# Optimization experiments

Measured on AMD Instinct MI355X. Metric: run time of the kernel, lower is better.

## Reference

```python
import jax, jax.numpy as jnp
import numpy as np

N = 50000      # nodes
E = 800000     # edges (avg degree 16)
F = 32         # n_features
FOUT = 32      # n_features_out
L = 2          # n_layers (Message+Update pairs)
LEN = 10.0     # length_scale


def _mlp(x, w1, b1, w2, b2):
    # embedding.MLP: Linear -> SiLU -> Linear
    return jax.nn.silu(x @ w1 + b1) @ w2 + b2


def _posenc(d):
    # sinusoidal PositionalEncoder(F, length=LEN): ranks 1..F/2
    ranks = jnp.arange(1, F // 2 + 1, dtype=d.dtype)
    a = d[:, None] * ranks * (jnp.pi / LEN)           # [E, F/2]
    return jnp.concatenate([jnp.sin(a), jnp.cos(a)], axis=-1)  # [E, F]


def _painn(s, v, edge_index, edge_dist, edge_dir,
           mp_w1, mp_b1, mp_w2, mp_b2, mw_w1, mw_b1, mw_w2, mw_b2,
           u_U, u_V, u_w1, u_b1, u_w2, u_b2,
           ro_w1, ro_b1, ro_w2, ro_b2, ro_V):
    src, dst = edge_index[0], edge_index[1]
    pe = _posenc(edge_dist)                            # [E, F]
    dirb = edge_dir[:, None, :]                        # [E, 1, 3]
    for l in range(L):
        # ---- Message ----
        mix = _mlp(s[src], mp_w1[l], mp_b1[l], mp_w2[l], mp_b2[l]) \
            * _mlp(pe, mw_w1[l], mw_b1[l], mw_w2[l], mw_b2[l])     # [E, 4F]
        gates, cpg, sed, sf = jnp.split(mix, 4, axis=-1)
        cross = jnp.cross(dirb, v[dst])                # [E, F, 3] (broadcast)
        dv = sed[:, :, None] * dirb + gates[:, :, None] * v[src] \
           + cpg[:, :, None] * cross                   # [E, F, 3]
        ds = sf * s[src]                               # [E, F]
        v = v + jax.ops.segment_sum(dv, dst, num_segments=N)
        s = s + jax.ops.segment_sum(ds, dst, num_segments=N)
        # ---- Update ----
        Vv = jnp.einsum('nfc,fg->ngc', v, u_V[l])      # [N, F, 3]
        Uv = jnp.einsum('nfc,fg->ngc', v, u_U[l])
        Vn = jnp.linalg.norm(Vv, axis=-1)              # [N, F]
        g, ssn, add = jnp.split(
            _mlp(jnp.concatenate([Vn, s], axis=-1), u_w1[l], u_b1[l], u_w2[l], u_b2[l]),
            3, axis=-1)
        v = v + g[:, :, None] * Uv
        s = s + Vn * Vn * ssn + add
    # ---- Readout ----
    inv_out, gates = jnp.split(_mlp(s, ro_w1, ro_b1, ro_w2, ro_b2), 2, axis=-1)
    eqv_out = gates[:, :, None] * jnp.einsum('nfc,fg->ngc', v, ro_V)
    return inv_out, eqv_out


def setup_inputs() -> dict:
    key = jax.random.key(0)
    ks = iter(jax.random.split(key, 64))
    nk = lambda: next(ks)
    lin = lambda fin, fout, *lead: (jax.random.normal(nk(), (*lead, fin, fout), jnp.float32)
                                    / np.sqrt(fin).astype(np.float32))
    d = {}
    d['invariant_node_features'] = jax.random.normal(nk(), (N, F), jnp.float32)
    d['equivariant_node_features'] = jax.random.normal(nk(), (N, F, 3), jnp.float32)
    d['edge_index'] = jax.random.randint(nk(), (2, E), 0, N)
    d['edge_dist'] = jax.random.uniform(nk(), (E,), jnp.float32) * LEN
    g = jax.random.normal(nk(), (E, 3), jnp.float32)
    d['edge_dir'] = g / jnp.linalg.norm(g, axis=-1, keepdims=True)
    # Message MLPs (phi on node features, W on positional encoding)
    d['mp_w1'] = lin(F, F, L); d['mp_b1'] = jnp.zeros((L, F), jnp.float32)
    d['mp_w2'] = lin(F, 4 * F, L); d['mp_b2'] = jnp.zeros((L, 4 * F), jnp.float32)
    d['mw_w1'] = lin(F, F, L); d['mw_b1'] = jnp.zeros((L, F), jnp.float32)
    d['mw_w2'] = lin(F, 4 * F, L); d['mw_b2'] = jnp.zeros((L, 4 * F), jnp.float32)
    # Update: EquivariantLinear U, V and MLP(2F -> F -> 3F)
    d['u_U'] = lin(F, F, L); d['u_V'] = lin(F, F, L)
    d['u_w1'] = lin(2 * F, F, L); d['u_b1'] = jnp.zeros((L, F), jnp.float32)
    d['u_w2'] = lin(F, 3 * F, L); d['u_b2'] = jnp.zeros((L, 3 * F), jnp.float32)
    # Readout: MLP(F -> F -> 2*FOUT) and EquivariantLinear V (F -> FOUT)
    d['ro_w1'] = lin(F, F); d['ro_b1'] = jnp.zeros((F,), jnp.float32)
    d['ro_w2'] = lin(F, 2 * FOUT); d['ro_b2'] = jnp.zeros((2 * FOUT,), jnp.float32)
    d['ro_V'] = lin(F, FOUT)
    return d


def reference(invariant_node_features, equivariant_node_features, edge_index,
              edge_dist, edge_dir,
              mp_w1, mp_b1, mp_w2, mp_b2, mw_w1, mw_b1, mw_w2, mw_b2,
              u_U, u_V, u_w1, u_b1, u_w2, u_b2,
              ro_w1, ro_b1, ro_w2, ro_b2, ro_V):
    return _painn(invariant_node_features, equivariant_node_features, edge_index,
                  edge_dist, edge_dir,
                  mp_w1, mp_b1, mp_w2, mp_b2, mw_w1, mw_b1, mw_w2, mw_b2,
                  u_U, u_V, u_w1, u_b1, u_w2, u_b2,
                  ro_w1, ro_b1, ro_w2, ro_b2, ro_V)
```

## Files before the change

kernel.cpp:

```cpp
#include <hip/hip_runtime.h>
#include <math.h>

#define PI_LEN 0.3141592653589793f
#define LEN_F  10.0f
#define TBL    4096

__device__ __forceinline__ float fsilu(float x) {
  return x * __builtin_amdgcn_rcpf(1.f + __expf(-x));
}

__global__ __launch_bounds__(256) void hist_kernel(const int* __restrict__ ei,
                                                   int* __restrict__ deg, int E_) {
  int e = blockIdx.x * 256 + threadIdx.x;
  if (e < E_) atomicAdd(&deg[ei[E_ + e]], 1);
}

__global__ __launch_bounds__(1024) void scan_kernel(const int* __restrict__ deg,
                                                    int* __restrict__ off,
                                                    int* __restrict__ cursor, int N_) {
  __shared__ int wtot[16];
  __shared__ int carry_s;
  int tid = threadIdx.x, lane = tid & 63, wid = tid >> 6;
  if (tid == 0) carry_s = 0;
  __syncthreads();
  int nch = (N_ + 8191) / 8192;
  for (int c = 0; c < nch; ++c) {
    int base_idx = c * 8192 + tid * 8;
    int x[8]; int mysum = 0;
    #pragma unroll
    for (int j = 0; j < 8; ++j) { int idx = base_idx + j; x[j] = (idx < N_) ? deg[idx] : 0; mysum += x[j]; }
    int incl = mysum;
    #pragma unroll
    for (int s = 1; s < 64; s <<= 1) { int t = __shfl_up(incl, s, 64); if (lane >= s) incl += t; }
    if (lane == 63) wtot[wid] = incl;
    __syncthreads();
    if (wid == 0) {
      int wt = (lane < 16) ? wtot[lane] : 0;
      #pragma unroll
      for (int s = 1; s < 16; s <<= 1) { int t = __shfl_up(wt, s, 64); if (lane >= s) wt += t; }
      if (lane < 16) wtot[lane] = wt;
    }
    __syncthreads();
    int wexcl = (wid > 0) ? wtot[wid - 1] : 0;
    int run = carry_s + wexcl + (incl - mysum);
    #pragma unroll
    for (int j = 0; j < 8; ++j) {
      int idx = base_idx + j;
      if (idx < N_) { off[idx] = run; cursor[idx] = run; }
      run += x[j];
    }
    __syncthreads();
    if (tid == 0) carry_s += wtot[15];
    __syncthreads();
  }
  if (tid == 0) off[N_] = carry_s;
}

__device__ __forceinline__ void mlp_tbl_block(
    int i, int g, int t,
    const float* __restrict__ w1, const float* __restrict__ b1,
    const float* __restrict__ w2, const float* __restrict__ b2,
    float4* __restrict__ tbl4, float (*pe)[96], float (*hl)[32])
{
  bool okt = (t <= TBL);
  float d = (float)t * (LEN_F / (float)TBL);
  pe[i][g] = (g < 16) ? __sinf(d * (float)(g + 1) * PI_LEN)
                      : __cosf(d * (float)(g - 15) * PI_LEN);
  float h = b1[g];
  for (int k = 0; k < 32; ++k) h += pe[i][k] * w1[k*32 + g];
  hl[i][g] = fsilu(h);
  float o0 = b2[g], o1 = b2[32+g], o2 = b2[64+g], o3 = b2[96+g];
  for (int k = 0; k < 32; ++k) {
    float hk = hl[i][k];
    o0 += hk * w2[k*128 +      g];
    o1 += hk * w2[k*128 + 32 + g];
    o2 += hk * w2[k*128 + 64 + g];
    o3 += hk * w2[k*128 + 96 + g];
  }
  if (okt) tbl4[(long)t*32 + g] = make_float4(o0, o1, o2, o3);
}

__global__ __launch_bounds__(256) void prep_kernel(
    const int* __restrict__ ei, const float* __restrict__ dist,
    const float* __restrict__ edir, int* __restrict__ cursor,
    int* __restrict__ srcp, float4* __restrict__ edata,
    const float* __restrict__ s,
    const float* __restrict__ mpw1, const float* __restrict__ mpb1,
    const float* __restrict__ mpw2, const float* __restrict__ mpb2,
    const float* __restrict__ mww1, const float* __restrict__ mwb1,
    const float* __restrict__ mww2, const float* __restrict__ mwb2,
    float4* __restrict__ Aout4, float4* __restrict__ tbl4,
    int N_, int E_, int edgeBlocks, int nodeBlocks)
{
  __shared__ float a[8][96];
  __shared__ float c[8][32];
  int bid = blockIdx.x;
  if (bid < edgeBlocks) {
    int e = bid * 256 + threadIdx.x;
    if (e < E_) {
      int dst = ei[E_ + e];
      int pos = atomicAdd(&cursor[dst], 1);
      srcp[pos] = ei[e];
      edata[pos] = make_float4(edir[3*e], edir[3*e+1], edir[3*e+2], dist[e]);
    }
    return;
  }
  bid -= edgeBlocks;
  int tid = threadIdx.x, i = tid >> 5, g = tid & 31;
  if (bid >= nodeBlocks) {
    int t = (bid - nodeBlocks) * 8 + i;
    mlp_tbl_block(i, g, t, mww1, mwb1, mww2, mwb2, tbl4, a, c);
    return;
  }
  long n = (long)bid * 8 + i;
  bool ok = (n < N_);
  a[i][g] = ok ? s[n*32 + g] : 0.f;
  float h = mpb1[g];
  for (int k = 0; k < 32; ++k) h += a[i][k] * mpw1[k*32 + g];
  c[i][g] = fsilu(h);
  float o0 = mpb2[g], o1 = mpb2[32+g], o2 = mpb2[64+g], o3 = mpb2[96+g];
  for (int k = 0; k < 32; ++k) {
    float hk = c[i][k];
    o0 += hk * mpw2[k*128 +      g];
    o1 += hk * mpw2[k*128 + 32 + g];
    o2 += hk * mpw2[k*128 + 64 + g];
    o3 += hk * mpw2[k*128 + 96 + g];
  }
  if (ok) Aout4[n*32 + g] = make_float4(o0, o1, o2, o3 * a[i][g]);
}

#define EDGE_MATH(ED, M0, M1, FR, Av, V0, V1, V2)                         \
  {                                                                        \
    float ga = M0.x + FR*(M1.x - M0.x);                                    \
    float ca = M0.y + FR*(M1.y - M0.y);                                    \
    float da = M0.z + FR*(M1.z - M0.z);                                    \
    float sa = M0.w + FR*(M1.w - M0.w);                                    \
    float gates = ga*Av.x, cpg = ca*Av.y, sed = da*Av.z;                   \
    acc_s += sa*Av.w;                                                      \
    float crx = ED.y*vd2 - ED.z*vd1;                                       \
    float cry = ED.z*vd0 - ED.x*vd2;                                       \
    float crz = ED.x*vd1 - ED.y*vd0;                                       \
    av0 += sed*ED.x + gates*V0 + cpg*crx;                                  \
    av1 += sed*ED.y + gates*V1 + cpg*cry;                                  \
    av2 += sed*ED.z + gates*V2 + cpg*crz;                                  \
  }

__global__ __launch_bounds__(256) void gather_kernel(
    const int* __restrict__ off, const int* __restrict__ srcp,
    const float4* __restrict__ edata, const float4* __restrict__ tbl4,
    const float* __restrict__ v_prev, const float4* __restrict__ Aout4,
    float4* __restrict__ acc4, int N_)
{
  int tid = threadIdx.x, w = tid >> 6, lane = tid & 63, g = lane & 31, hf = lane >> 5;
  int n = blockIdx.x * 4 + w;
  if (n >= N_) return;
  const float* vp = v_prev + (long)n*96 + g*3;
  float vd0 = vp[0], vd1 = vp[1], vd2 = vp[2];
  int pstart = off[n], pend = off[n + 1];
  float acc_s = 0, av0 = 0, av1 = 0, av2 = 0;
  const float inv_step = (float)TBL / LEN_F;

  int deg = pend - pstart;
  int nfull = deg >> 3;
  int pb = pstart + hf * 4;
  for (int it = 0; it < nfull; ++it, pb += 8) {
    int srcs[4]; float4 ed[4];
    #pragma unroll
    for (int b = 0; b < 4; ++b) { srcs[b] = srcp[pb + b]; ed[b] = edata[pb + b]; }
    float4 m0[4], m1[4], A[4]; float fr[4];
    float vs0[4], vs1[4], vs2[4];
    #pragma unroll
    for (int b = 0; b < 4; ++b) {
      float x = ed[b].w * inv_step;
      float f = floorf(x);
      int i0 = (int)f; if (i0 > TBL - 1) i0 = TBL - 1;
      fr[b] = x - f;
      m0[b] = tbl4[(long)i0*32 + g];
      m1[b] = tbl4[(long)(i0 + 1)*32 + g];
      A[b]  = Aout4[(long)srcs[b]*32 + g];
      const float* vq = v_prev + (long)srcs[b]*96 + g*3;
      vs0[b] = vq[0]; vs1[b] = vq[1]; vs2[b] = vq[2];
    }
    #pragma unroll
    for (int b = 0; b < 4; ++b)
      EDGE_MATH(ed[b], m0[b], m1[b], fr[b], A[b], vs0[b], vs1[b], vs2[b]);
  }
  int p = pstart + nfull * 8 + hf;
  for (; p + 2 < pend; p += 4) {
    int  s0_ = srcp[p], s1_ = srcp[p + 2];
    float4 e0 = edata[p], e1 = edata[p + 2];
    float x0 = e0.w * inv_step, x1 = e1.w * inv_step;
    float f0 = floorf(x0), f1 = floorf(x1);
    int i0 = (int)f0; if (i0 > TBL - 1) i0 = TBL - 1;
    int i1 = (int)f1; if (i1 > TBL - 1) i1 = TBL - 1;
    float r0 = x0 - f0, r1 = x1 - f1;
    float4 a0 = tbl4[(long)i0*32 + g], b0 = tbl4[(long)(i0+1)*32 + g];
    float4 a1 = tbl4[(long)i1*32 + g], b1 = tbl4[(long)(i1+1)*32 + g];
    float4 A0 = Aout4[(long)s0_*32 + g], A1 = Aout4[(long)s1_*32 + g];
    const float* vq0 = v_prev + (long)s0_*96 + g*3;
    const float* vq1 = v_prev + (long)s1_*96 + g*3;
    float u0 = vq0[0], u1 = vq0[1], u2 = vq0[2];
    float t0 = vq1[0], t1 = vq1[1], t2 = vq1[2];
    EDGE_MATH(e0, a0, b0, r0, A0, u0, u1, u2);
    EDGE_MATH(e1, a1, b1, r1, A1, t0, t1, t2);
  }
  if (p < pend) {
    int  s0_ = srcp[p];
    float4 e0 = edata[p];
    float x0 = e0.w * inv_step;
    float f0 = floorf(x0);
    int i0 = (int)f0; if (i0 > TBL - 1) i0 = TBL - 1;
    float r0 = x0 - f0;
    float4 a0 = tbl4[(long)i0*32 + g], b0 = tbl4[(long)(i0+1)*32 + g];
    float4 A0 = Aout4[(long)s0_*32 + g];
    const float* vq0 = v_prev + (long)s0_*96 + g*3;
    float u0 = vq0[0], u1 = vq0[1], u2 = vq0[2];
    EDGE_MATH(e0, a0, b0, r0, A0, u0, u1, u2);
  }
  av0   += __shfl_xor(av0, 32);
  av1   += __shfl_xor(av1, 32);
  av2   += __shfl_xor(av2, 32);
  acc_s += __shfl_xor(acc_s, 32);
  if (hf == 0) acc4[(long)n*32 + g] = make_float4(av0, av1, av2, acc_s);
}

__global__ __launch_bounds__(256) void update_mid_kernel(
    const float* __restrict__ s_prev, const float* __restrict__ v_prev,
    const float4* __restrict__ acc4,
    const float* __restrict__ uU, const float* __restrict__ uV,
    const float* __restrict__ uw1, const float* __restrict__ ub1,
    const float* __restrict__ uw2, const float* __restrict__ ub2,
    const float* __restrict__ nw1, const float* __restrict__ nb1,
    const float* __restrict__ nw2, const float* __restrict__ nb2,
    const float* __restrict__ tw1, const float* __restrict__ tb1,
    const float* __restrict__ tw2, const float* __restrict__ tb2,
    float* __restrict__ s_out, float* __restrict__ v_out,
    float4* __restrict__ Aout4, float4* __restrict__ tbl4,
    int N_, int nodeBlocks)
{
  __shared__ float vld[8][96];
  __shared__ float in64[8][64];
  __shared__ float hld[8][32];
  int tid = threadIdx.x, i = tid >> 5, g = tid & 31;
  if (blockIdx.x >= nodeBlocks) {
    int t = (blockIdx.x - nodeBlocks) * 8 + i;
    mlp_tbl_block(i, g, t, tw1, tb1, tw2, tb2, tbl4, vld, hld);
    return;
  }
  long n = (long)blockIdx.x * 8 + i;
  bool ok = (n < N_);
  float nv0 = 0, nv1 = 0, nv2 = 0, ns = 0;
  if (ok) {
    float4 a = acc4[n*32 + g];
    const float* vp = v_prev + n*96 + g*3;
    nv0 = vp[0] + a.x; nv1 = vp[1] + a.y; nv2 = vp[2] + a.z;
    ns  = s_prev[n*32 + g] + a.w;
  }
  vld[i][g*3+0] = nv0; vld[i][g*3+1] = nv1; vld[i][g*3+2] = nv2;
  float Vv0=0,Vv1=0,Vv2=0,Uv0=0,Uv1=0,Uv2=0;
  for (int f = 0; f < 32; ++f) {
    float wu = uU[f*32 + g];
    float wv = uV[f*32 + g];
    float v0 = vld[i][f*3+0], v1 = vld[i][f*3+1], v2 = vld[i][f*3+2];
    Vv0 += v0*wv; Vv1 += v1*wv; Vv2 += v2*wv;
    Uv0 += v0*wu; Uv1 += v1*wu; Uv2 += v2*wu;
  }
  float Vn = sqrtf(Vv0*Vv0 + Vv1*Vv1 + Vv2*Vv2);
  in64[i][g] = Vn; in64[i][32 + g] = ns;
  float h = ub1[g];
  for (int k = 0; k < 64; ++k) h += in64[i][k] * uw1[k*32 + g];
  h = fsilu(h);
  hld[i][g] = h;
  float og = ub2[g], ossn = ub2[32 + g], oadd = ub2[64 + g];
  for (int k = 0; k < 32; ++k) {
    float hk = hld[i][k];
    og   += hk * uw2[k*96 +      g];
    ossn += hk * uw2[k*96 + 32 + g];
    oadd += hk * uw2[k*96 + 64 + g];
  }
  float s_fin = ns + Vn*Vn*ossn + oadd;
  if (ok) {
    float* vo = v_out + n*96 + g*3;
    vo[0] = nv0 + og*Uv0;
    vo[1] = nv1 + og*Uv1;
    vo[2] = nv2 + og*Uv2;
    s_out[n*32 + g] = s_fin;
  }
  in64[i][g] = s_fin;
  float h2 = nb1[g];
  for (int k = 0; k < 32; ++k) h2 += in64[i][k] * nw1[k*32 + g];
  h2 = fsilu(h2);
  hld[i][g] = h2;
  float o0 = nb2[g], o1 = nb2[32+g], o2 = nb2[64+g], o3 = nb2[96+g];
  for (int k = 0; k < 32; ++k) {
    float hk = hld[i][k];
    o0 += hk * nw2[k*128 +      g];
    o1 += hk * nw2[k*128 + 32 + g];
    o2 += hk * nw2[k*128 + 64 + g];
    o3 += hk * nw2[k*128 + 96 + g];
  }
  if (ok) Aout4[n*32 + g] = make_float4(o0, o1, o2, o3 * s_fin);
}

__global__ __launch_bounds__(256) void update_final_kernel(
    const float* __restrict__ s_prev, const float* __restrict__ v_prev,
    const float4* __restrict__ acc4,
    const float* __restrict__ uU, const float* __restrict__ uV,
    const float* __restrict__ uw1, const float* __restrict__ ub1,
    const float* __restrict__ uw2, const float* __restrict__ ub2,
    const float* __restrict__ rw1, const float* __restrict__ rb1,
    const float* __restrict__ rw2, const float* __restrict__ rb2,
    const float* __restrict__ roV, float* __restrict__ out, int N_)
{
  __shared__ float vld[8][96];
  __shared__ float in64[8][64];
  __shared__ float hld[8][32];
  int tid = threadIdx.x, i = tid >> 5, g = tid & 31;
  long n = (long)blockIdx.x * 8 + i;
  bool ok = (n < N_);
  float nv0 = 0, nv1 = 0, nv2 = 0, ns = 0;
  if (ok) {
    float4 a = acc4[n*32 + g];
    const float* vp = v_prev + n*96 + g*3;
    nv0 = vp[0] + a.x; nv1 = vp[1] + a.y; nv2 = vp[2] + a.z;
    ns  = s_prev[n*32 + g] + a.w;
  }
  vld[i][g*3+0] = nv0; vld[i][g*3+1] = nv1; vld[i][g*3+2] = nv2;
  float Vv0=0,Vv1=0,Vv2=0,Uv0=0,Uv1=0,Uv2=0;
  for (int f = 0; f < 32; ++f) {
    float wu = uU[f*32 + g];
    float wv = uV[f*32 + g];
    float v0 = vld[i][f*3+0], v1 = vld[i][f*3+1], v2 = vld[i][f*3+2];
    Vv0 += v0*wv; Vv1 += v1*wv; Vv2 += v2*wv;
    Uv0 += v0*wu; Uv1 += v1*wu; Uv2 += v2*wu;
  }
  float Vn = sqrtf(Vv0*Vv0 + Vv1*Vv1 + Vv2*Vv2);
  in64[i][g] = Vn; in64[i][32 + g] = ns;
  float h = ub1[g];
  for (int k = 0; k < 64; ++k) h += in64[i][k] * uw1[k*32 + g];
  h = fsilu(h);
  hld[i][g] = h;
  float og = ub2[g], ossn = ub2[32 + g], oadd = ub2[64 + g];
  for (int k = 0; k < 32; ++k) {
    float hk = hld[i][k];
    og   += hk * uw2[k*96 +      g];
    ossn += hk * uw2[k*96 + 32 + g];
    oadd += hk * uw2[k*96 + 64 + g];
  }
  float s_fin = ns + Vn*Vn*ossn + oadd;
  float vf0 = nv0 + og*Uv0, vf1 = nv1 + og*Uv1, vf2 = nv2 + og*Uv2;
  in64[i][g] = s_fin;
  float h2 = rb1[g];
  for (int k = 0; k < 32; ++k) h2 += in64[i][k] * rw1[k*32 + g];
  h2 = fsilu(h2);
  hld[i][g] = h2;
  float inv = rb2[g], gate = rb2[32 + g];
  for (int k = 0; k < 32; ++k) {
    float hk = hld[i][k];
    inv  += hk * rw2[k*64 +      g];
    gate += hk * rw2[k*64 + 32 + g];
  }
  vld[i][g*3+0] = vf0; vld[i][g*3+1] = vf1; vld[i][g*3+2] = vf2;
  float R0 = 0, R1 = 0, R2 = 0;
  for (int f = 0; f < 32; ++f) {
    float wv = roV[f*32 + g];
    R0 += vld[i][f*3+0]*wv; R1 += vld[i][f*3+1]*wv; R2 += vld[i][f*3+2]*wv;
  }
  if (ok) {
    out[n*32 + g] = inv;
    long eb = (long)N_*32 + n*96 + (long)g*3;
    out[eb+0] = gate*R0; out[eb+1] = gate*R1; out[eb+2] = gate*R2;
  }
}

extern "C" void kernel_launch(void* const* d_in, const int* in_sizes, int n_in,
                              void* d_out, int out_size, void* d_ws, size_t ws_size,
                              hipStream_t stream)
{
  const float* s_in  = (const float*)d_in[0];
  const float* v_in  = (const float*)d_in[1];
  const int*   ei    = (const int*)  d_in[2];
  const float* dist  = (const float*)d_in[3];
  const float* edir  = (const float*)d_in[4];
  const float* mp_w1 = (const float*)d_in[5];
  const float* mp_b1 = (const float*)d_in[6];
  const float* mp_w2 = (const float*)d_in[7];
  const float* mp_b2 = (const float*)d_in[8];
  const float* mw_w1 = (const float*)d_in[9];
  const float* mw_b1 = (const float*)d_in[10];
  const float* mw_w2 = (const float*)d_in[11];
  const float* mw_b2 = (const float*)d_in[12];
  const float* u_U   = (const float*)d_in[13];
  const float* u_V   = (const float*)d_in[14];
  const float* u_w1  = (const float*)d_in[15];
  const float* u_b1  = (const float*)d_in[16];
  const float* u_w2  = (const float*)d_in[17];
  const float* u_b2  = (const float*)d_in[18];
  const float* ro_w1 = (const float*)d_in[19];
  const float* ro_b1 = (const float*)d_in[20];
  const float* ro_w2 = (const float*)d_in[21];
  const float* ro_b2 = (const float*)d_in[22];
  const float* ro_V  = (const float*)d_in[23];

  int N_ = in_sizes[0] / 32;
  int E_ = in_sizes[3];

  float*  sB    = (float*)d_ws;
  float*  vB    = sB + (size_t)N_*32;
  float4* Aout4 = (float4*)(vB + (size_t)N_*96);
  float4* acc4b = Aout4 + (size_t)N_*32;
  float4* tbl4  = acc4b + (size_t)N_*32;
  float4* edata = tbl4 + (size_t)(TBL+1)*32;
  int*    srcp  = (int*)(edata + (size_t)E_);
  int*    deg   = srcp + E_;
  int*    off   = deg + N_;
  int*    cursor= off + N_ + 1;

  float4* acc4a = (float4*)d_out;

  int nodeBlocks = (N_ + 7) / 8;
  int gathBlocks = (N_ + 3) / 4;
  int edgeBlocks = (E_ + 255) / 256;
  int tblBlocks  = (TBL + 1 + 7) / 8;

  hipMemsetAsync(deg, 0, (size_t)N_ * sizeof(int), stream);
  hist_kernel<<<edgeBlocks, 256, 0, stream>>>(ei, deg, E_);
  scan_kernel<<<1, 1024, 0, stream>>>(deg, off, cursor, N_);

  prep_kernel<<<edgeBlocks + nodeBlocks + tblBlocks, 256, 0, stream>>>(
      ei, dist, edir, cursor, srcp, edata,
      s_in, mp_w1, mp_b1, mp_w2, mp_b2, mw_w1, mw_b1, mw_w2, mw_b2,
      Aout4, tbl4, N_, E_, edgeBlocks, nodeBlocks);

  gather_kernel<<<gathBlocks, 256, 0, stream>>>(
      off, srcp, edata, tbl4, v_in, Aout4, acc4a, N_);

  update_mid_kernel<<<nodeBlocks + tblBlocks, 256, 0, stream>>>(
      s_in, v_in, acc4a,
      u_U, u_V, u_w1, u_b1, u_w2, u_b2,
      mp_w1 + 1024, mp_b1 + 32, mp_w2 + 4096, mp_b2 + 128,
      mw_w1 + 1024, mw_b1 + 32, mw_w2 + 4096, mw_b2 + 128,
      sB, vB, Aout4, tbl4, N_, nodeBlocks);

  gather_kernel<<<gathBlocks, 256, 0, stream>>>(
      off, srcp, edata, tbl4, vB, Aout4, acc4b, N_);

  update_final_kernel<<<nodeBlocks, 256, 0, stream>>>(
      sB, vB, acc4b,
      u_U + 1024, u_V + 1024, u_w1 + 2048, u_b1 + 32, u_w2 + 3072, u_b2 + 96,
      ro_w1, ro_b1, ro_w2, ro_b2, ro_V, (float*)d_out, N_);
}
```

Measured before the change: 632.7 us.

## Merge scan with node/table prep, split scatter, split update K-loops across half-waves

Folds the single-block degree scan into a 1024-thread kernel that also runs the layer-0 node MLP and builds both layers' positional-encoding MLP tables, so the lone scan block overlaps with that independent work. Edge scatter into CSR order becomes its own kernel after the scan. The update kernels now give each node a 64-lane wave, with the two half-waves splitting each reduction and combining via xor shuffles, which shortens the serial dot-product chains. The cost is duplicate loads in the second half-wave and separate table and Aout buffers per layer.

Result: faster. 611.3 us (-3.4%).

```diff
diff --git a/kernel.cpp b/kernel.cpp
--- a/kernel.cpp
+++ b/kernel.cpp
@@ -15,52 +15,11 @@
   if (e < E_) atomicAdd(&deg[ei[E_ + e]], 1);
 }
 
-__global__ __launch_bounds__(1024) void scan_kernel(const int* __restrict__ deg,
-                                                    int* __restrict__ off,
-                                                    int* __restrict__ cursor, int N_) {
-  __shared__ int wtot[16];
-  __shared__ int carry_s;
-  int tid = threadIdx.x, lane = tid & 63, wid = tid >> 6;
-  if (tid == 0) carry_s = 0;
-  __syncthreads();
-  int nch = (N_ + 8191) / 8192;
-  for (int c = 0; c < nch; ++c) {
-    int base_idx = c * 8192 + tid * 8;
-    int x[8]; int mysum = 0;
-    #pragma unroll
-    for (int j = 0; j < 8; ++j) { int idx = base_idx + j; x[j] = (idx < N_) ? deg[idx] : 0; mysum += x[j]; }
-    int incl = mysum;
-    #pragma unroll
-    for (int s = 1; s < 64; s <<= 1) { int t = __shfl_up(incl, s, 64); if (lane >= s) incl += t; }
-    if (lane == 63) wtot[wid] = incl;
-    __syncthreads();
-    if (wid == 0) {
-      int wt = (lane < 16) ? wtot[lane] : 0;
-      #pragma unroll
-      for (int s = 1; s < 16; s <<= 1) { int t = __shfl_up(wt, s, 64); if (lane >= s) wt += t; }
-      if (lane < 16) wtot[lane] = wt;
-    }
-    __syncthreads();
-    int wexcl = (wid > 0) ? wtot[wid - 1] : 0;
-    int run = carry_s + wexcl + (incl - mysum);
-    #pragma unroll
-    for (int j = 0; j < 8; ++j) {
-      int idx = base_idx + j;
-      if (idx < N_) { off[idx] = run; cursor[idx] = run; }
-      run += x[j];
-    }
-    __syncthreads();
-    if (tid == 0) carry_s += wtot[15];
-    __syncthreads();
-  }
-  if (tid == 0) off[N_] = carry_s;
-}
-
-__device__ __forceinline__ void mlp_tbl_block(
+__device__ __forceinline__ void tbl_role(
     int i, int g, int t,
     const float* __restrict__ w1, const float* __restrict__ b1,
     const float* __restrict__ w2, const float* __restrict__ b2,
-    float4* __restrict__ tbl4, float (*pe)[96], float (*hl)[32])
+    float4* __restrict__ tbl4, float (*pe)[32], float (*hl)[32])
 {
   bool okt = (t <= TBL);
   float d = (float)t * (LEN_F / (float)TBL);
@@ -80,53 +39,102 @@
   if (okt) tbl4[(long)t*32 + g] = make_float4(o0, o1, o2, o3);
 }
 
-__global__ __launch_bounds__(256) void prep_kernel(
-    const int* __restrict__ ei, const float* __restrict__ dist,
-    const float* __restrict__ edir, int* __restrict__ cursor,
-    int* __restrict__ srcp, float4* __restrict__ edata,
+__global__ __launch_bounds__(1024) void scan_prep_kernel(
+    const int* __restrict__ deg, int* __restrict__ off,
+    int* __restrict__ cursor, int N_,
     const float* __restrict__ s,
     const float* __restrict__ mpw1, const float* __restrict__ mpb1,
     const float* __restrict__ mpw2, const float* __restrict__ mpb2,
-    const float* __restrict__ mww1, const float* __restrict__ mwb1,
-    const float* __restrict__ mww2, const float* __restrict__ mwb2,
-    float4* __restrict__ Aout4, float4* __restrict__ tbl4,
-    int N_, int E_, int edgeBlocks, int nodeBlocks)
-{
-  __shared__ float a[8][96];
-  __shared__ float c[8][32];
+    const float* __restrict__ mww1a, const float* __restrict__ mwb1a,
+    const float* __restrict__ mww2a, const float* __restrict__ mwb2a,
+    const float* __restrict__ mww1b, const float* __restrict__ mwb1b,
+    const float* __restrict__ mww2b, const float* __restrict__ mwb2b,
+    float4* __restrict__ Aout4a, float4* __restrict__ tbl4a,
+    float4* __restrict__ tbl4b, int nodeB32, int tblB32)
+{
+  __shared__ float xs[32][32];
+  __shared__ float hs[32][32];
+  __shared__ int wtot[16];
+  __shared__ int carry_s;
   int bid = blockIdx.x;
-  if (bid < edgeBlocks) {
-    int e = bid * 256 + threadIdx.x;
-    if (e < E_) {
-      int dst = ei[E_ + e];
-      int pos = atomicAdd(&cursor[dst], 1);
-      srcp[pos] = ei[e];
-      edata[pos] = make_float4(edir[3*e], edir[3*e+1], edir[3*e+2], dist[e]);
+  int tid = threadIdx.x;
+  if (bid == 0) {
+    int lane = tid & 63, wid = tid >> 6;
+    if (tid == 0) carry_s = 0;
+    __syncthreads();
+    int nch = (N_ + 8191) / 8192;
+    for (int c = 0; c < nch; ++c) {
+      int base_idx = c * 8192 + tid * 8;
+      int x[8]; int mysum = 0;
+      #pragma unroll
+      for (int j = 0; j < 8; ++j) { int idx = base_idx + j; x[j] = (idx < N_) ? deg[idx] : 0; mysum += x[j]; }
+      int incl = mysum;
+      #pragma unroll
+      for (int st = 1; st < 64; st <<= 1) { int t = __shfl_up(incl, st, 64); if (lane >= st) incl += t; }
+      if (lane == 63) wtot[wid] = incl;
+      __syncthreads();
+      if (wid == 0) {
+        int wt = (lane < 16) ? wtot[lane] : 0;
+        #pragma unroll
+        for (int st = 1; st < 16; st <<= 1) { int t = __shfl_up(wt, st, 64); if (lane >= st) wt += t; }
+        if (lane < 16) wtot[lane] = wt;
+      }
+      __syncthreads();
+      int wexcl = (wid > 0) ? wtot[wid - 1] : 0;
+      int run = carry_s + wexcl + (incl - mysum);
+      #pragma unroll
+      for (int j = 0; j < 8; ++j) {
+        int idx = base_idx + j;
+        if (idx < N_) { off[idx] = run; cursor[idx] = run; }
+        run += x[j];
+      }
+      __syncthreads();
+      if (tid == 0) carry_s += wtot[15];
+      __syncthreads();
     }
+    if (tid == 0) off[N_] = carry_s;
     return;
   }
-  bid -= edgeBlocks;
-  int tid = threadIdx.x, i = tid >> 5, g = tid & 31;
-  if (bid >= nodeBlocks) {
-    int t = (bid - nodeBlocks) * 8 + i;
-    mlp_tbl_block(i, g, t, mww1, mwb1, mww2, mwb2, tbl4, a, c);
+  bid -= 1;
+  int i = tid >> 5, g = tid & 31;
+  if (bid < nodeB32) {
+    long n = (long)bid * 32 + i;
+    bool ok = (n < N_);
+    xs[i][g] = ok ? s[n*32 + g] : 0.f;
+    float h = mpb1[g];
+    for (int k = 0; k < 32; ++k) h += xs[i][k] * mpw1[k*32 + g];
+    hs[i][g] = fsilu(h);
+    float o0 = mpb2[g], o1 = mpb2[32+g], o2 = mpb2[64+g], o3 = mpb2[96+g];
+    for (int k = 0; k < 32; ++k) {
+      float hk = hs[i][k];
+      o0 += hk * mpw2[k*128 +      g];
+      o1 += hk * mpw2[k*128 + 32 + g];
+      o2 += hk * mpw2[k*128 + 64 + g];
+      o3 += hk * mpw2[k*128 + 96 + g];
+    }
+    if (ok) Aout4a[n*32 + g] = make_float4(o0, o1, o2, o3 * xs[i][g]);
     return;
   }
-  long n = (long)bid * 8 + i;
-  bool ok = (n < N_);
-  a[i][g] = ok ? s[n*32 + g] : 0.f;
-  float h = mpb1[g];
-  for (int k = 0; k < 32; ++k) h += a[i][k] * mpw1[k*32 + g];
-  c[i][g] = fsilu(h);
-  float o0 = mpb2[g], o1 = mpb2[32+g], o2 = mpb2[64+g], o3 = mpb2[96+g];
-  for (int k = 0; k < 32; ++k) {
-    float hk = c[i][k];
-    o0 += hk * mpw2[k*128 +      g];
-    o1 += hk * mpw2[k*128 + 32 + g];
-    o2 += hk * mpw2[k*128 + 64 + g];
-    o3 += hk * mpw2[k*128 + 96 + g];
-  }
-  if (ok) Aout4[n*32 + g] = make_float4(o0, o1, o2, o3 * a[i][g]);
+  bid -= nodeB32;
+  if (bid < tblB32) {
+    tbl_role(i, g, bid * 32 + i, mww1a, mwb1a, mww2a, mwb2a, tbl4a, xs, hs);
+    return;
+  }
+  bid -= tblB32;
+  tbl_role(i, g, bid * 32 + i, mww1b, mwb1b, mww2b, mwb2b, tbl4b, xs, hs);
+}
+
+__global__ __launch_bounds__(256) void scatter_kernel(
+    const int* __restrict__ ei, const float* __restrict__ dist,
+    const float* __restrict__ edir, int* __restrict__ cursor,
+    int* __restrict__ srcp, float4* __restrict__ edata, int E_) {
+  int e = blockIdx.x * 256 + threadIdx.x;
+  if (e < E_) {
+    int dst = ei[E_ + e];
+    int pos = atomicAdd(&cursor[dst], 1);
+    srcp[pos] = ei[e];
+    edata[pos] = make_float4(edir[3*e], edir[3*e+1], edir[3*e+2], dist[e]);
+  }
 }
 
 #define EDGE_MATH(ED, M0, M1, FR, Av, V0, V1, V2)                         \
@@ -232,77 +240,86 @@
     const float* __restrict__ uw2, const float* __restrict__ ub2,
     const float* __restrict__ nw1, const float* __restrict__ nb1,
     const float* __restrict__ nw2, const float* __restrict__ nb2,
-    const float* __restrict__ tw1, const float* __restrict__ tb1,
-    const float* __restrict__ tw2, const float* __restrict__ tb2,
     float* __restrict__ s_out, float* __restrict__ v_out,
-    float4* __restrict__ Aout4, float4* __restrict__ tbl4,
-    int N_, int nodeBlocks)
-{
-  __shared__ float vld[8][96];
-  __shared__ float in64[8][64];
-  __shared__ float hld[8][32];
-  int tid = threadIdx.x, i = tid >> 5, g = tid & 31;
-  if (blockIdx.x >= nodeBlocks) {
-    int t = (blockIdx.x - nodeBlocks) * 8 + i;
-    mlp_tbl_block(i, g, t, tw1, tb1, tw2, tb2, tbl4, vld, hld);
-    return;
-  }
-  long n = (long)blockIdx.x * 8 + i;
-  bool ok = (n < N_);
-  float nv0 = 0, nv1 = 0, nv2 = 0, ns = 0;
-  if (ok) {
-    float4 a = acc4[n*32 + g];
-    const float* vp = v_prev + n*96 + g*3;
-    nv0 = vp[0] + a.x; nv1 = vp[1] + a.y; nv2 = vp[2] + a.z;
-    ns  = s_prev[n*32 + g] + a.w;
-  }
-  vld[i][g*3+0] = nv0; vld[i][g*3+1] = nv1; vld[i][g*3+2] = nv2;
+    float4* __restrict__ Aout4b, int N_)
+{
+  __shared__ float vld[4][96];
+  __shared__ float in64[4][64];
+  __shared__ float hld[4][32];
+  int tid = threadIdx.x, w = tid >> 6, lane = tid & 63, g = lane & 31, hf = lane >> 5;
+  long n = (long)blockIdx.x * 4 + w;
+  if (n >= N_) return;
+  float4 a = acc4[n*32 + g];
+  const float* vp = v_prev + n*96 + g*3;
+  float nv0 = vp[0] + a.x, nv1 = vp[1] + a.y, nv2 = vp[2] + a.z;
+  float ns  = s_prev[n*32 + g] + a.w;
+  if (hf == 0) { vld[w][g*3+0] = nv0; vld[w][g*3+1] = nv1; vld[w][g*3+2] = nv2; }
   float Vv0=0,Vv1=0,Vv2=0,Uv0=0,Uv1=0,Uv2=0;
-  for (int f = 0; f < 32; ++f) {
+  for (int j = 0; j < 16; ++j) {
+    int f = hf * 16 + j;
     float wu = uU[f*32 + g];
     float wv = uV[f*32 + g];
-    float v0 = vld[i][f*3+0], v1 = vld[i][f*3+1], v2 = vld[i][f*3+2];
+    float v0 = vld[w][f*3+0], v1 = vld[w][f*3+1], v2 = vld[w][f*3+2];
     Vv0 += v0*wv; Vv1 += v1*wv; Vv2 += v2*wv;
     Uv0 += v0*wu; Uv1 += v1*wu; Uv2 += v2*wu;
   }
+  Vv0 += __shfl_xor(Vv0, 32); Vv1 += __shfl_xor(Vv1, 32); Vv2 += __shfl_xor(Vv2, 32);
+  Uv0 += __shfl_xor(Uv0, 32); Uv1 += __shfl_xor(Uv1, 32); Uv2 += __shfl_xor(Uv2, 32);
   float Vn = sqrtf(Vv0*Vv0 + Vv1*Vv1 + Vv2*Vv2);
-  in64[i][g] = Vn; in64[i][32 + g] = ns;
-  float h = ub1[g];
-  for (int k = 0; k < 64; ++k) h += in64[i][k] * uw1[k*32 + g];
-  h = fsilu(h);
-  hld[i][g] = h;
-  float og = ub2[g], ossn = ub2[32 + g], oadd = ub2[64 + g];
-  for (int k = 0; k < 32; ++k) {
-    float hk = hld[i][k];
+  if (hf == 0) { in64[w][g] = Vn; in64[w][32 + g] = ns; }
+  float h = 0.f;
+  for (int j = 0; j < 32; ++j) {
+    int k = hf * 32 + j;
+    h += in64[w][k] * uw1[k*32 + g];
+  }
+  h += __shfl_xor(h, 32);
+  h = fsilu(h + ub1[g]);
+  if (hf == 0) hld[w][g] = h;
+  float og = 0.f, ossn = 0.f, oadd = 0.f;
+  for (int j = 0; j < 16; ++j) {
+    int k = hf * 16 + j;
+    float hk = hld[w][k];
     og   += hk * uw2[k*96 +      g];
     ossn += hk * uw2[k*96 + 32 + g];
     oadd += hk * uw2[k*96 + 64 + g];
   }
+  og   += __shfl_xor(og, 32);
+  ossn += __shfl_xor(ossn, 32);
+  oadd += __shfl_xor(oadd, 32);
+  og += ub2[g]; ossn += ub2[32 + g]; oadd += ub2[64 + g];
   float s_fin = ns + Vn*Vn*ossn + oadd;
-  if (ok) {
+  if (hf == 0) {
     float* vo = v_out + n*96 + g*3;
     vo[0] = nv0 + og*Uv0;
     vo[1] = nv1 + og*Uv1;
     vo[2] = nv2 + og*Uv2;
     s_out[n*32 + g] = s_fin;
   }
-  in64[i][g] = s_fin;
-  float h2 = nb1[g];
-  for (int k = 0; k < 32; ++k) h2 += in64[i][k] * nw1[k*32 + g];
-  h2 = fsilu(h2);
-  hld[i][g] = h2;
-  float o0 = nb2[g], o1 = nb2[32+g], o2 = nb2[64+g], o3 = nb2[96+g];
-  for (int k = 0; k < 32; ++k) {
-    float hk = hld[i][k];
+  if (hf == 0) in64[w][g] = s_fin;
+  float h2 = 0.f;
+  for (int j = 0; j < 16; ++j) {
+    int k = hf * 16 + j;
+    h2 += in64[w][k] * nw1[k*32 + g];
+  }
+  h2 += __shfl_xor(h2, 32);
+  h2 = fsilu(h2 + nb1[g]);
+  if (hf == 0) hld[w][g] = h2;
+  float o0 = 0.f, o1 = 0.f, o2 = 0.f, o3 = 0.f;
+  for (int j = 0; j < 16; ++j) {
+    int k = hf * 16 + j;
+    float hk = hld[w][k];
     o0 += hk * nw2[k*128 +      g];
     o1 += hk * nw2[k*128 + 32 + g];
     o2 += hk * nw2[k*128 + 64 + g];
     o3 += hk * nw2[k*128 + 96 + g];
   }
-  if (ok) Aout4[n*32 + g] = make_float4(o0, o1, o2, o3 * s_fin);
-}
-
-__global__ __launch_bounds__(256) void update_final_kernel(
+  o0 += __shfl_xor(o0, 32); o1 += __shfl_xor(o1, 32);
+  o2 += __shfl_xor(o2, 32); o3 += __shfl_xor(o3, 32);
+  o0 += nb2[g]; o1 += nb2[32+g]; o2 += nb2[64+g]; o3 += nb2[96+g];
+  if (hf == 0) Aout4b[n*32 + g] = make_float4(o0, o1, o2, o3 * s_fin);
+}
+
+__global__ __launch_bounds__(256) void update_fin_kernel(
     const float* __restrict__ s_prev, const float* __restrict__ v_prev,
     const float4* __restrict__ acc4,
     const float* __restrict__ uU, const float* __restrict__ uV,
@@ -312,61 +329,80 @@
     const float* __restrict__ rw2, const float* __restrict__ rb2,
     const float* __restrict__ roV, float* __restrict__ out, int N_)
 {
-  __shared__ float vld[8][96];
-  __shared__ float in64[8][64];
-  __shared__ float hld[8][32];
-  int tid = threadIdx.x, i = tid >> 5, g = tid & 31;
-  long n = (long)blockIdx.x * 8 + i;
-  bool ok = (n < N_);
-  float nv0 = 0, nv1 = 0, nv2 = 0, ns = 0;
-  if (ok) {
-    float4 a = acc4[n*32 + g];
-    const float* vp = v_prev + n*96 + g*3;
-    nv0 = vp[0] + a.x; nv1 = vp[1] + a.y; nv2 = vp[2] + a.z;
-    ns  = s_prev[n*32 + g] + a.w;
-  }
-  vld[i][g*3+0] = nv0; vld[i][g*3+1] = nv1; vld[i][g*3+2] = nv2;
+  __shared__ float vld[4][96];
+  __shared__ float in64[4][64];
+  __shared__ float hld[4][32];
+  int tid = threadIdx.x, w = tid >> 6, lane = tid & 63, g = lane & 31, hf = lane >> 5;
+  long n = (long)blockIdx.x * 4 + w;
+  if (n >= N_) return;
+  float4 a = acc4[n*32 + g];
+  const float* vp = v_prev + n*96 + g*3;
+  float nv0 = vp[0] + a.x, nv1 = vp[1] + a.y, nv2 = vp[2] + a.z;
+  float ns  = s_prev[n*32 + g] + a.w;
+  if (hf == 0) { vld[w][g*3+0] = nv0; vld[w][g*3+1] = nv1; vld[w][g*3+2] = nv2; }
   float Vv0=0,Vv1=0,Vv2=0,Uv0=0,Uv1=0,Uv2=0;
-  for (int f = 0; f < 32; ++f) {
+  for (int j = 0; j < 16; ++j) {
+    int f = hf * 16 + j;
     float wu = uU[f*32 + g];
     float wv = uV[f*32 + g];
-    float v0 = vld[i][f*3+0], v1 = vld[i][f*3+1], v2 = vld[i][f*3+2];
+    float v0 = vld[w][f*3+0], v1 = vld[w][f*3+1], v2 = vld[w][f*3+2];
     Vv0 += v0*wv; Vv1 += v1*wv; Vv2 += v2*wv;
     Uv0 += v0*wu; Uv1 += v1*wu; Uv2 += v2*wu;
   }
+  Vv0 += __shfl_xor(Vv0, 32); Vv1 += __shfl_xor(Vv1, 32); Vv2 += __shfl_xor(Vv2, 32);
+  Uv0 += __shfl_xor(Uv0, 32); Uv1 += __shfl_xor(Uv1, 32); Uv2 += __shfl_xor(Uv2, 32);
   float Vn = sqrtf(Vv0*Vv0 + Vv1*Vv1 + Vv2*Vv2);
-  in64[i][g] = Vn; in64[i][32 + g] = ns;
-  float h = ub1[g];
-  for (int k = 0; k < 64; ++k) h += in64[i][k] * uw1[k*32 + g];
-  h = fsilu(h);
-  hld[i][g] = h;
-  float og = ub2[g], ossn = ub2[32 + g], oadd = ub2[64 + g];
-  for (int k = 0; k < 32; ++k) {
-    float hk = hld[i][k];
+  if (hf == 0) { in64[w][g] = Vn; in64[w][32 + g] = ns; }
+  float h = 0.f;
+  for (int j = 0; j < 32; ++j) {
+    int k = hf * 32 + j;
+    h += in64[w][k] * uw1[k*32 + g];
+  }
+  h += __shfl_xor(h, 32);
+  h = fsilu(h + ub1[g]);
+  if (hf == 0) hld[w][g] = h;
+  float og = 0.f, ossn = 0.f, oadd = 0.f;
+  for (int j = 0; j < 16; ++j) {
+    int k = hf * 16 + j;
+    float hk = hld[w][k];
     og   += hk * uw2[k*96 +      g];
     ossn += hk * uw2[k*96 + 32 + g];
     oadd += hk * uw2[k*96 + 64 + g];
   }
+  og   += __shfl_xor(og, 32);
+  ossn += __shfl_xor(ossn, 32);
+  oadd += __shfl_xor(oadd, 32);
+  og += ub2[g]; ossn += ub2[32 + g]; oadd += ub2[64 + g];
   float s_fin = ns + Vn*Vn*ossn + oadd;
   float vf0 = nv0 + og*Uv0, vf1 = nv1 + og*Uv1, vf2 = nv2 + og*Uv2;
-  in64[i][g] = s_fin;
-  float h2 = rb1[g];
-  for (int k = 0; k < 32; ++k) h2 += in64[i][k] * rw1[k*32 + g];
-  h2 = fsilu(h2);
-  hld[i][g] = h2;
-  float inv = rb2[g], gate = rb2[32 + g];
-  for (int k = 0; k < 32; ++k) {
-    float hk = hld[i][k];
+  if (hf == 0) in64[w][g] = s_fin;
+  float h2 = 0.f;
+  for (int j = 0; j < 16; ++j) {
+    int k = hf * 16 + j;
+    h2 += in64[w][k] * rw1[k*32 + g];
+  }
+  h2 += __shfl_xor(h2, 32);
+  h2 = fsilu(h2 + rb1[g]);
+  if (hf == 0) hld[w][g] = h2;
+  float inv = 0.f, gate = 0.f;
+  for (int j = 0; j < 16; ++j) {
+    int k = hf * 16 + j;
+    float hk = hld[w][k];
     inv  += hk * rw2[k*64 +      g];
     gate += hk * rw2[k*64 + 32 + g];
   }
-  vld[i][g*3+0] = vf0; vld[i][g*3+1] = vf1; vld[i][g*3+2] = vf2;
+  inv  += __shfl_xor(inv, 32);
+  gate += __shfl_xor(gate, 32);
+  inv += rb2[g]; gate += rb2[32 + g];
+  if (hf == 0) { vld[w][g*3+0] = vf0; vld[w][g*3+1] = vf1; vld[w][g*3+2] = vf2; }
   float R0 = 0, R1 = 0, R2 = 0;
-  for (int f = 0; f < 32; ++f) {
+  for (int j = 0; j < 16; ++j) {
+    int f = hf * 16 + j;
     float wv = roV[f*32 + g];
-    R0 += vld[i][f*3+0]*wv; R1 += vld[i][f*3+1]*wv; R2 += vld[i][f*3+2]*wv;
-  }
-  if (ok) {
+    R0 += vld[w][f*3+0]*wv; R1 += vld[w][f*3+1]*wv; R2 += vld[w][f*3+2]*wv;
+  }
+  R0 += __shfl_xor(R0, 32); R1 += __shfl_xor(R1, 32); R2 += __shfl_xor(R2, 32);
+  if (hf == 0) {
     out[n*32 + g] = inv;
     long eb = (long)N_*32 + n*96 + (long)g*3;
     out[eb+0] = gate*R0; out[eb+1] = gate*R1; out[eb+2] = gate*R2;
@@ -407,10 +443,12 @@
 
   float*  sB    = (float*)d_ws;
   float*  vB    = sB + (size_t)N_*32;
-  float4* Aout4 = (float4*)(vB + (size_t)N_*96);
-  float4* acc4b = Aout4 + (size_t)N_*32;
-  float4* tbl4  = acc4b + (size_t)N_*32;
-  float4* edata = tbl4 + (size_t)(TBL+1)*32;
+  float4* Aout4a= (float4*)(vB + (size_t)N_*96);
+  float4* Aout4b= Aout4a + (size_t)N_*32;
+  float4* acc4b = Aout4b + (size_t)N_*32;
+  float4* tbl4a = acc4b + (size_t)N_*32;
+  float4* tbl4b = tbl4a + (size_t)(TBL+1)*32;
+  float4* edata = tbl4b + (size_t)(TBL+1)*32;
   int*    srcp  = (int*)(edata + (size_t)E_);
   int*    deg   = srcp + E_;
   int*    off   = deg + N_;
@@ -418,34 +456,35 @@
 
   float4* acc4a = (float4*)d_out;
 
-  int nodeBlocks = (N_ + 7) / 8;
   int gathBlocks = (N_ + 3) / 4;
+  int updBlocks  = (N_ + 3) / 4;
   int edgeBlocks = (E_ + 255) / 256;
-  int tblBlocks  = (TBL + 1 + 7) / 8;
+  int nodeB32    = (N_ + 31) / 32;
+  int tblB32     = (TBL + 1 + 31) / 32;
 
   hipMemsetAsync(deg, 0, (size_t)N_ * sizeof(int), stream);
   hist_kernel<<<edgeBlocks, 256, 0, stream>>>(ei, deg, E_);
-  scan_kernel<<<1, 1024, 0, stream>>>(deg, off, cursor, N_);
-
-  prep_kernel<<<edgeBlocks + nodeBlocks + tblBlocks, 256, 0, stream>>>(
-      ei, dist, edir, cursor, srcp, edata,
-      s_in, mp_w1, mp_b1, mp_w2, mp_b2, mw_w1, mw_b1, mw_w2, mw_b2,
-      Aout4, tbl4, N_, E_, edgeBlocks, nodeBlocks);
+
+  scan_prep_kernel<<<1 + nodeB32 + 2*tblB32, 1024, 0, stream>>>(
+      deg, off, cursor, N_, s_in,
+      mp_w1, mp_b1, mp_w2, mp_b2,
+      mw_w1, mw_b1, mw_w2, mw_b2,
+      mw_w1 + 1024, mw_b1 + 32, mw_w2 + 4096, mw_b2 + 128,
+      Aout4a, tbl4a, tbl4b, nodeB32, tblB32);
+
+  scatter_kernel<<<edgeBlocks, 256, 0, stream>>>(ei, dist, edir, cursor, srcp, edata, E_);
 
   gather_kernel<<<gathBlocks, 256, 0, stream>>>(
-      off, srcp, edata, tbl4, v_in, Aout4, acc4a, N_);
-
-  update_mid_kernel<<<nodeBlocks + tblBlocks, 256, 0, stream>>>(
+      off, srcp, edata, tbl4a, v_in, Aout4a, acc4a, N_);
+  update_mid_kernel<<<updBlocks, 256, 0, stream>>>(
       s_in, v_in, acc4a,
       u_U, u_V, u_w1, u_b1, u_w2, u_b2,
       mp_w1 + 1024, mp_b1 + 32, mp_w2 + 4096, mp_b2 + 128,
-      mw_w1 + 1024, mw_b1 + 32, mw_w2 + 4096, mw_b2 + 128,
-      sB, vB, Aout4, tbl4, N_, nodeBlocks);
+      sB, vB, Aout4b, N_);
 
   gather_kernel<<<gathBlocks, 256, 0, stream>>>(
-      off, srcp, edata, tbl4, vB, Aout4, acc4b, N_);
-
-  update_final_kernel<<<nodeBlocks, 256, 0, stream>>>(
+      off, srcp, edata, tbl4b, vB, Aout4b, acc4b, N_);
+  update_fin_kernel<<<updBlocks, 256, 0, stream>>>(
       sB, vB, acc4b,
       u_U + 1024, u_V + 1024, u_w1 + 2048, u_b1 + 32, u_w2 + 3072, u_b2 + 96,
       ro_w1, ro_b1, ro_w2, ro_b2, ro_V, (float*)d_out, N_);
```
